# Kernel tuning notes

Hardware: AMD Instinct MI355X
Metric: run time of the kernel (lower is better)

Reference implementation:

```python
import jax, jax.numpy as jnp
import numpy as np

MAX_SHIFT = 1  # kernel width = 2*MAX_SHIFT + 1 = 3


def setup_inputs() -> dict:
    key = jax.random.key(0)
    ks = jax.random.split(key, 7)
    B, N, M = 256, 4096, 64
    return {
        "memory": jax.random.normal(ks[0], (B, N, M), dtype=jnp.float32),
        "k": jax.random.normal(ks[1], (B, M), dtype=jnp.float32),
        "beta": jax.random.uniform(ks[2], (B, 1), dtype=jnp.float32),
        "prev_w": jax.random.uniform(ks[3], (B, N), dtype=jnp.float32),
        "g": jax.random.uniform(ks[4], (B, 1), dtype=jnp.float32),
        "s": jax.random.uniform(ks[5], (B, 2 * MAX_SHIFT + 1), dtype=jnp.float32),
        "gamma": jax.random.uniform(ks[6], (B, 1), dtype=jnp.float32),
    }


def reference(memory, k, beta, prev_w, g, s, gamma):
    eps = 1e-8
    # content addressing: cosine similarity of k against each memory row
    dot = jnp.einsum("bm,bnm->bn", k, memory)                      # [B,N]
    k_norm = jnp.maximum(jnp.linalg.norm(k, axis=1, keepdims=True), eps)   # [B,1]
    m_norm = jnp.maximum(jnp.linalg.norm(memory, axis=2), eps)             # [B,N]
    sim = dot / (k_norm * m_norm)
    w_c = jax.nn.softmax(beta * sim, axis=1)                       # [B,N]
    # gated interpolation
    w_g = g * w_c + (1.0 - g) * prev_w                             # [B,N]
    # circular shift: per-row correlation with kernel s (equivalent to the
    # original BxB conv1d + diagonal extraction)
    S = MAX_SHIFT
    N = w_g.shape[1]
    unrolled = jnp.concatenate([w_g[:, -S:], w_g, w_g[:, :S]], axis=1)  # [B,N+2S]
    windows = jnp.stack([unrolled[:, i:i + N] for i in range(2 * S + 1)], axis=1)  # [B,2S+1,N]
    w_s = jnp.einsum("bi,bin->bn", s, windows)                     # [B,N]
    # sharpen + normalize
    w_pow = w_s ** gamma
    return w_pow / (jnp.sum(w_pow, axis=1, keepdims=True) + 1e-16)
```

## Files before the change

### kernel.cpp

```cpp
#include <hip/hip_runtime.h>
#include <math.h>

#define NN 4096
#define MM 64
#define THREADS 1024

__device__ __forceinline__ float wave_red_sum(float v) {
#pragma unroll
    for (int o = 32; o > 0; o >>= 1) v += __shfl_down(v, o, 64);
    return v;
}
__device__ __forceinline__ float wave_red_max(float v) {
#pragma unroll
    for (int o = 32; o > 0; o >>= 1) v = fmaxf(v, __shfl_down(v, o, 64));
    return v;
}

__device__ __forceinline__ float block_sum(float v, float* scratch) {
    const int tid = threadIdx.x;
    const int lane = tid & 63, wid = tid >> 6;
    v = wave_red_sum(v);
    if (lane == 0) scratch[wid] = v;
    __syncthreads();
    if (tid < 64) {
        float x = (tid < 16) ? scratch[tid] : 0.0f;
        x = wave_red_sum(x);
        if (tid == 0) scratch[16] = x;
    }
    __syncthreads();
    float r = scratch[16];
    __syncthreads();
    return r;
}
__device__ __forceinline__ float block_max(float v, float* scratch) {
    const int tid = threadIdx.x;
    const int lane = tid & 63, wid = tid >> 6;
    v = wave_red_max(v);
    if (lane == 0) scratch[wid] = v;
    __syncthreads();
    if (tid < 64) {
        float x = (tid < 16) ? scratch[tid] : -INFINITY;
        x = wave_red_max(x);
        if (tid == 0) scratch[16] = x;
    }
    __syncthreads();
    float r = scratch[16];
    __syncthreads();
    return r;
}

extern "C" __global__ void __launch_bounds__(THREADS)
ntm_head_kernel(const float* __restrict__ memory, const float* __restrict__ k,
                const float* __restrict__ beta, const float* __restrict__ prev_w,
                const float* __restrict__ g, const float* __restrict__ s,
                const float* __restrict__ gamma, float* __restrict__ out) {
    __shared__ float dotA[NN];
    __shared__ float sqA[NN];
    __shared__ float wg[NN];
    __shared__ float kk[MM];
    __shared__ float scratch[32];
    __shared__ float knorm_sh;

    const int b = blockIdx.x;
    const int tid = threadIdx.x;
    const float* __restrict__ memB = memory + (size_t)b * NN * MM;

    if (tid < MM) kk[tid] = k[b * MM + tid];
    __syncthreads();

    if (tid < 64) {
        float kv2 = kk[tid] * kk[tid];
        float sk = wave_red_sum(kv2);
        if (tid == 0) knorm_sh = fmaxf(sqrtf(sk), 1e-8f);
    }

    const int m4 = (tid & 15) * 4;
    const float kx = kk[m4], ky = kk[m4 + 1], kz = kk[m4 + 2], kw = kk[m4 + 3];

#pragma unroll 4
    for (int it = 0; it < 64; ++it) {
        const float4 mv = *(const float4*)(memB + (size_t)it * 4096 + tid * 4);
        float d = mv.x * kx + mv.y * ky + mv.z * kz + mv.w * kw;
        float q = mv.x * mv.x + mv.y * mv.y + mv.z * mv.z + mv.w * mv.w;
#pragma unroll
        for (int o = 8; o >= 1; o >>= 1) {
            d += __shfl_down(d, o, 16);
            q += __shfl_down(q, o, 16);
        }
        if ((tid & 15) == 0) {
            const int n = it * 64 + (tid >> 4);
            dotA[n] = d;
            sqA[n] = q;
        }
    }
    __syncthreads();

    const float knorm = knorm_sh;
    const float beta_b = beta[b];
    const float g_b = g[b];
    const float s0 = s[b * 3], s1 = s[b * 3 + 1], s2 = s[b * 3 + 2];
    const float gamma_b = gamma[b];

    float val[4];
    float lmax = -INFINITY;
#pragma unroll
    for (int j = 0; j < 4; ++j) {
        const int n = tid + j * THREADS;
        const float mn = fmaxf(sqrtf(sqA[n]), 1e-8f);
        const float v = beta_b * (dotA[n] / (knorm * mn));
        val[j] = v;
        lmax = fmaxf(lmax, v);
    }
    const float mx = block_max(lmax, scratch);

    float e[4];
    float lsum = 0.0f;
#pragma unroll
    for (int j = 0; j < 4; ++j) {
        e[j] = expf(val[j] - mx);
        lsum += e[j];
    }
    const float sumE = block_sum(lsum, scratch);

#pragma unroll
    for (int j = 0; j < 4; ++j) {
        const int n = tid + j * THREADS;
        const float wc = e[j] / sumE;
        const float pw = prev_w[(size_t)b * NN + n];
        wg[n] = g_b * wc + (1.0f - g_b) * pw;
    }
    __syncthreads();

    float wp[4];
    float lsum2 = 0.0f;
#pragma unroll
    for (int j = 0; j < 4; ++j) {
        const int n = tid + j * THREADS;
        const int nm = (n + NN - 1) & (NN - 1);
        const int np_ = (n + 1) & (NN - 1);
        const float ws = s0 * wg[nm] + s1 * wg[n] + s2 * wg[np_];
        const float p = (float)pow((double)ws, (double)gamma_b);
        wp[j] = p;
        lsum2 += p;
    }
    const float sumP = block_sum(lsum2, scratch);
    const float denom = sumP + 1e-16f;
#pragma unroll
    for (int j = 0; j < 4; ++j) {
        const int n = tid + j * THREADS;
        out[(size_t)b * NN + n] = wp[j] / denom;
    }
}

extern "C" void kernel_launch(void* const* d_in, const int* in_sizes, int n_in,
                              void* d_out, int out_size, void* d_ws, size_t ws_size,
                              hipStream_t stream) {
    const float* memory = (const float*)d_in[0];
    const float* k      = (const float*)d_in[1];
    const float* beta   = (const float*)d_in[2];
    const float* prev_w = (const float*)d_in[3];
    const float* g      = (const float*)d_in[4];
    const float* s      = (const float*)d_in[5];
    const float* gamma  = (const float*)d_in[6];
    float* out = (float*)d_out;

    const int B = in_sizes[2];
    ntm_head_kernel<<<B, THREADS, 0, stream>>>(memory, k, beta, prev_w, g, s, gamma, out);
}
```

Measured before the change: 377.2 us.

## Compute per-row dot and norm in registers, one thread per memory row

Each thread now owns four memory rows and accumulates the dot product and squared norm over all 64 columns in registers. This removes the 16-lane shuffle reductions and the shared-memory dotA/sqA arrays plus their barrier, and prev_w is loaded up front. The price is uncoalesced access: each thread walks its own 256-byte row, so neighbouring lanes hit addresses 256 bytes apart on every load, which may hurt DRAM and cache efficiency on a memory-bound kernel.

Result: slower. 486.8 us (+29.1%).

```diff
diff --git a/kernel.cpp b/kernel.cpp
--- a/kernel.cpp
+++ b/kernel.cpp
@@ -54,10 +54,8 @@
                 const float* __restrict__ beta, const float* __restrict__ prev_w,
                 const float* __restrict__ g, const float* __restrict__ s,
                 const float* __restrict__ gamma, float* __restrict__ out) {
-    __shared__ float dotA[NN];
-    __shared__ float sqA[NN];
+    __shared__ __align__(16) float kk[MM];
     __shared__ float wg[NN];
-    __shared__ float kk[MM];
     __shared__ float scratch[32];
     __shared__ float knorm_sh;
 
@@ -65,49 +63,45 @@
     const int tid = threadIdx.x;
     const float* __restrict__ memB = memory + (size_t)b * NN * MM;
 
-    if (tid < MM) kk[tid] = k[b * MM + tid];
-    __syncthreads();
-
-    if (tid < 64) {
-        float kv2 = kk[tid] * kk[tid];
-        float sk = wave_red_sum(kv2);
-        if (tid == 0) knorm_sh = fmaxf(sqrtf(sk), 1e-8f);
-    }
-
-    const int m4 = (tid & 15) * 4;
-    const float kx = kk[m4], ky = kk[m4 + 1], kz = kk[m4 + 2], kw = kk[m4 + 3];
-
-#pragma unroll 4
-    for (int it = 0; it < 64; ++it) {
-        const float4 mv = *(const float4*)(memB + (size_t)it * 4096 + tid * 4);
-        float d = mv.x * kx + mv.y * ky + mv.z * kz + mv.w * kw;
-        float q = mv.x * mv.x + mv.y * mv.y + mv.z * mv.z + mv.w * mv.w;
+    float pw[4];
 #pragma unroll
-        for (int o = 8; o >= 1; o >>= 1) {
-            d += __shfl_down(d, o, 16);
-            q += __shfl_down(q, o, 16);
-        }
-        if ((tid & 15) == 0) {
-            const int n = it * 64 + (tid >> 4);
-            dotA[n] = d;
-            sqA[n] = q;
-        }
-    }
-    __syncthreads();
-
-    const float knorm = knorm_sh;
+    for (int j = 0; j < 4; ++j)
+        pw[j] = prev_w[(size_t)b * NN + tid + j * THREADS];
     const float beta_b = beta[b];
     const float g_b = g[b];
     const float s0 = s[b * 3], s1 = s[b * 3 + 1], s2 = s[b * 3 + 2];
     const float gamma_b = gamma[b];
 
+    if (tid < 64) {
+        const float kv = k[b * MM + tid];
+        kk[tid] = kv;
+        const float sk = wave_red_sum(kv * kv);
+        if (tid == 0) knorm_sh = fmaxf(sqrtf(sk), 1e-8f);
+    }
+    __syncthreads();
+
+    float d[4] = {0.f, 0.f, 0.f, 0.f};
+    float q[4] = {0.f, 0.f, 0.f, 0.f};
+    const float* base = memB + (size_t)tid * MM;
+#pragma unroll
+    for (int i = 0; i < 16; ++i) {
+        const float4 kf = *(const float4*)(kk + i * 4);
+#pragma unroll
+        for (int j = 0; j < 4; ++j) {
+            const float4 mv = *(const float4*)(base + (size_t)j * THREADS * MM + i * 4);
+            d[j] += mv.x * kf.x + mv.y * kf.y + mv.z * kf.z + mv.w * kf.w;
+            q[j] += mv.x * mv.x + mv.y * mv.y + mv.z * mv.z + mv.w * mv.w;
+        }
+    }
+
+    const float knorm = knorm_sh;
+
     float val[4];
     float lmax = -INFINITY;
 #pragma unroll
     for (int j = 0; j < 4; ++j) {
-        const int n = tid + j * THREADS;
-        const float mn = fmaxf(sqrtf(sqA[n]), 1e-8f);
-        const float v = beta_b * (dotA[n] / (knorm * mn));
+        const float mn = fmaxf(sqrtf(q[j]), 1e-8f);
+        const float v = beta_b * (d[j] / (knorm * mn));
         val[j] = v;
         lmax = fmaxf(lmax, v);
     }
@@ -126,8 +120,7 @@
     for (int j = 0; j < 4; ++j) {
         const int n = tid + j * THREADS;
         const float wc = e[j] / sumE;
-        const float pw = prev_w[(size_t)b * NN + n];
-        wg[n] = g_b * wc + (1.0f - g_b) * pw;
+        wg[n] = g_b * wc + (1.0f - g_b) * pw[j];
     }
     __syncthreads();
 
```
